# Kernel tuning notes

Hardware: AMD Instinct MI355X
Metric: run time of the kernel (lower is better)

## Reference

```python
import jax, jax.numpy as jnp
import numpy as np

B, S, D, H = 4, 2048, 1024, 16
DK = D // H


def setup_inputs() -> dict:
    key = jax.random.key(0)
    kx, kq, kk, kv, ko = jax.random.split(key, 5)
    scale = D ** -0.5
    return {
        "x": jax.random.normal(kx, (B, S, D), dtype=jnp.float32),
        "W_q": jax.random.normal(kq, (D, D), dtype=jnp.float32) * scale,
        "W_k": jax.random.normal(kk, (D, D), dtype=jnp.float32) * scale,
        "W_v": jax.random.normal(kv, (D, D), dtype=jnp.float32) * scale,
        "W_o": jax.random.normal(ko, (D, D), dtype=jnp.float32) * scale,
    }


def reference(x, W_q, W_k, W_v, W_o):
    b, s, d = x.shape
    # projections: x @ W.T  (weights stored [out, in])
    def proj(W):
        return (x @ W.T).reshape(b, s, H, DK).transpose(0, 2, 1, 3)  # [b,h,s,dk]
    Q, K, V = proj(W_q), proj(W_k), proj(W_v)
    scores = jnp.einsum('bhqd,bhkd->bhqk', Q, K) * (DK ** -0.5)
    causal = jnp.tril(jnp.ones((s, s), dtype=bool))
    scores = jnp.where(causal, scores, -jnp.inf)
    attn = jax.nn.softmax(scores, axis=-1)
    out = jnp.einsum('bhqk,bhkd->bhqd', attn, V)  # [b,h,s,dk]
    out = out.transpose(0, 2, 1, 3).reshape(b, s, d)
    return out @ W_o.T
```

## Files before the change

kernel.cpp:

```cpp
#include <hip/hip_runtime.h>
#include <stdint.h>

#define B_ 4
#define S_ 2048
#define D_ 1024
#define H_ 16
#define DK_ 64
#define M_ (B_*S_)

typedef __attribute__((ext_vector_type(8))) short bhalf8;
typedef __attribute__((ext_vector_type(4))) short bhalf4;
typedef __attribute__((ext_vector_type(4))) float floatx4;
typedef unsigned short bfu;
typedef unsigned int u32;

__device__ __forceinline__ bfu f2bf(float f) {
  union { float f; u32 u; } v; v.f = f;
  u32 r = v.u + 0x7FFFu + ((v.u >> 16) & 1u);
  return (bfu)(r >> 16);
}

__device__ __forceinline__ u32 cvtpk(float a, float b) {
  u32 r;
  asm("v_cvt_pk_bf16_f32 %0, %1, %2" : "=v"(r) : "v"(a), "v"(b));
  return r;
}

__device__ __forceinline__ void gll16(const bfu* g, bfu* l) {
  __builtin_amdgcn_global_load_lds((__attribute__((address_space(1))) void*)g,
                                   (__attribute__((address_space(3))) void*)l,
                                   16, 0, 0);
}

__global__ void cvt_all(const float* __restrict__ x,  const float* __restrict__ wq,
                        const float* __restrict__ wk, const float* __restrict__ wv,
                        const float* __restrict__ wo, bfu* __restrict__ dst) {
  const size_t u = ((size_t)blockIdx.x * blockDim.x + threadIdx.x) * 4;
  const size_t XN = (size_t)M_ * D_;
  const float* src;
  if (u < XN) {
    src = x + u;
  } else {
    const size_t v = u - XN;
    const int wsel = (int)(v >> 20);
    const size_t off = v & ((size_t)(1u << 20) - 1);
    src = ((wsel == 0) ? wq : (wsel == 1) ? wk : (wsel == 2) ? wv : wo) + off;
  }
  float4 vv = *(const float4*)src;
  ushort4 o;
  o.x = f2bf(vv.x); o.y = f2bf(vv.y); o.z = f2bf(vv.z); o.w = f2bf(vv.w);
  *(ushort4*)(dst + u) = o;
}

__device__ __forceinline__ void gemm_core_gll(const bfu* __restrict__ A,
                                              const bfu* __restrict__ Bw,
                                              bfu* aT, bfu* bT,
                                              int m0, int bn0,
                                              floatx4 (&acc)[4][4])
{
  const int tid  = threadIdx.x;
  const int lane = tid & 63;
  const int g    = lane >> 4;
  const int i16  = lane & 15;
  const int w    = tid >> 6;
  const int wm   = w >> 1, wn = w & 1;

  const int lrow = lane >> 3;
  const int scol = ((lane & 7) ^ lrow) << 3;
  const bfu* As = A  + (size_t)(m0  + w * 32 + lrow) * D_ + scol;
  const bfu* Bs = Bw + (size_t)(bn0 + w * 32 + lrow) * D_ + scol;

  for (int k0 = 0; k0 < D_; k0 += 64) {
#pragma unroll
    for (int j = 0; j < 4; ++j) {
      gll16(As + (size_t)j * 8 * D_ + k0, aT + (w * 4 + j) * 512);
      gll16(Bs + (size_t)j * 8 * D_ + k0, bT + (w * 4 + j) * 512);
    }
    __syncthreads();
    const char* aTc = (const char*)aT;
    const char* bTc = (const char*)bT;
#pragma unroll
    for (int kb = 0; kb < 2; ++kb) {
      bhalf8 af[4], bf[4];
#pragma unroll
      for (int f = 0; f < 4; ++f) {
        int arow = wm * 64 + f * 16 + i16;
        af[f] = *(const bhalf8*)(aTc + arow * 128 + ((kb * 64 + g * 16) ^ ((arow & 7) << 4)));
        int brow = wn * 64 + f * 16 + i16;
        bf[f] = *(const bhalf8*)(bTc + brow * 128 + ((kb * 64 + g * 16) ^ ((brow & 7) << 4)));
      }
#pragma unroll
      for (int fm = 0; fm < 4; ++fm)
#pragma unroll
        for (int fn = 0; fn < 4; ++fn)
          acc[fm][fn] = __builtin_amdgcn_mfma_f32_16x16x32_bf16(af[fm], bf[fn], acc[fm][fn], 0, 0, 0);
    }
    __syncthreads();
  }
}

__global__ __launch_bounds__(256) void qkv_gemm(const bfu* __restrict__ xb,
                                                const bfu* __restrict__ wqkv,
                                                bfu* __restrict__ Qd,
                                                bfu* __restrict__ Kd,
                                                bfu* __restrict__ Vtd)
{
  __shared__ bfu aT[8192], bT[8192];
  const int bid = blockIdx.x;
  const int wi   = bid >> 3;
  const int xblk = wi >> 3;
  const int y    = ((bid & 7) << 3) | (wi & 7);
  const int m0   = y * 128;
  const int z    = xblk >> 3;
  const int n0   = (xblk & 7) * 128;
  const int bn0  = xblk * 128;

  floatx4 acc[4][4] = {};
  gemm_core_gll(xb, wqkv, aT, bT, m0, bn0, acc);

  bfu* dst = (z == 0) ? Qd : (z == 1) ? Kd : Vtd;
  const int lane = threadIdx.x & 63;
  const int g = lane >> 4, i16 = lane & 15;
  const int w = threadIdx.x >> 6, wm = w >> 1, wn = w & 1;
#pragma unroll
  for (int fm = 0; fm < 4; ++fm) {
#pragma unroll
    for (int fn = 0; fn < 4; ++fn) {
      int col = n0 + wn * 64 + fn * 16 + i16;
      int h = col >> 6, dk = col & 63;
#pragma unroll
      for (int r = 0; r < 4; ++r) {
        int mrow = m0 + wm * 64 + fm * 16 + g * 4 + r;
        int b = mrow >> 11, s = mrow & (S_ - 1);
        size_t idx = (z == 2)
            ? ((size_t)((b * H_ + h) * DK_ + dk)) * S_ + s
            : ((size_t)((b * H_ + h) * S_ + s)) * DK_ + dk;
        dst[idx] = f2bf(acc[fm][fn][r]);
      }
    }
  }
}

__global__ __launch_bounds__(256) void out_gemm(const bfu* __restrict__ Ab,
                                                const bfu* __restrict__ wob,
                                                float* __restrict__ out)
{
  __shared__ bfu aT[8192], bT[8192];
  const int bid = blockIdx.x;
  const int wi   = bid >> 3;
  const int xblk = wi >> 3;
  const int y    = ((bid & 7) << 3) | (wi & 7);
  const int m0   = y * 128;
  const int n0   = xblk * 128;

  floatx4 acc[4][4] = {};
  gemm_core_gll(Ab, wob, aT, bT, m0, n0, acc);

  const int lane = threadIdx.x & 63;
  const int g = lane >> 4, i16 = lane & 15;
  const int w = threadIdx.x >> 6, wm = w >> 1, wn = w & 1;
#pragma unroll
  for (int fm = 0; fm < 4; ++fm)
#pragma unroll
    for (int fn = 0; fn < 4; ++fn) {
      int col = n0 + wn * 64 + fn * 16 + i16;
#pragma unroll
      for (int r = 0; r < 4; ++r) {
        int mrow = m0 + wm * 64 + fm * 16 + g * 4 + r;
        out[(size_t)mrow * D_ + col] = acc[fm][fn][r];
      }
    }
}

template<int BUF>
__device__ __forceinline__ void attn_tile(const char* smem, int t, int ntw, int qr,
                                          int koff0, int koff1, const int (&voff)[4],
                                          bhalf8 qa0, bhalf8 qa1, int g, int i16,
                                          floatx4 (&ot)[4], float& mC2, float& lp)
{
  const float C2 = 0.125f * 1.44269504f;
  floatx4 sa[4] = {};
#pragma unroll
  for (int cb = 0; cb < 4; ++cb) {
    bhalf8 kf0 = *(const bhalf8*)(smem + BUF + cb * 2048 + koff0);
    bhalf8 kf1 = *(const bhalf8*)(smem + BUF + cb * 2048 + koff1);
    sa[cb] = __builtin_amdgcn_mfma_f32_16x16x32_bf16(kf0, qa0, sa[cb], 0, 0, 0);
    sa[cb] = __builtin_amdgcn_mfma_f32_16x16x32_bf16(kf1, qa1, sa[cb], 0, 0, 0);
  }
  if (t == ntw - 1) {
    const int kv0 = t * 64;
#pragma unroll
    for (int cb = 0; cb < 4; ++cb)
#pragma unroll
      for (int r = 0; r < 4; ++r)
        if (kv0 + cb * 16 + g * 4 + r > qr + i16) sa[cb][r] = -3.0e38f;
  }
  float pm = sa[0][0];
#pragma unroll
  for (int cb = 0; cb < 4; ++cb)
#pragma unroll
    for (int r = 0; r < 4; ++r)
      pm = fmaxf(pm, sa[cb][r]);
  pm = fmaxf(pm, __shfl_xor(pm, 16));
  pm = fmaxf(pm, __shfl_xor(pm, 32));
  const float pmC2 = pm * C2;
  if (!__all(pmC2 - mC2 <= 8.0f)) {
    const float nmax = fmaxf(mC2, pmC2);
    const float al = exp2f(mC2 - nmax);
    mC2 = nmax;
    lp *= al;
#pragma unroll
    for (int da = 0; da < 4; ++da)
#pragma unroll
      for (int r = 0; r < 4; ++r)
        ot[da][r] *= al;
  }
  const float nm = -mC2;
  u32 pk[8];
  float ps = 0.f;
#pragma unroll
  for (int cb = 0; cb < 4; ++cb) {
    float p0 = exp2f(__builtin_fmaf(sa[cb][0], C2, nm));
    float p1 = exp2f(__builtin_fmaf(sa[cb][1], C2, nm));
    float p2 = exp2f(__builtin_fmaf(sa[cb][2], C2, nm));
    float p3 = exp2f(__builtin_fmaf(sa[cb][3], C2, nm));
    ps += (p0 + p1) + (p2 + p3);
    pk[cb * 2]     = cvtpk(p0, p1);
    pk[cb * 2 + 1] = cvtpk(p2, p3);
  }
  lp += ps;
#pragma unroll
  for (int da = 0; da < 4; ++da) {
#pragma unroll
    for (int cb = 0; cb < 4; ++cb) {
      bhalf4 vf = *(const bhalf4*)(smem + BUF + voff[cb] + da * 2048);
      union { u32 u[2]; bhalf4 h; } pu;
      pu.u[0] = pk[cb * 2]; pu.u[1] = pk[cb * 2 + 1];
      ot[da] = __builtin_amdgcn_mfma_f32_16x16x16bf16_1k(vf, pu.h, ot[da], 0, 0, 0);
    }
  }
}

__global__ __launch_bounds__(512, 4) void attn_kernel(const bfu* __restrict__ Q,
                                                      const bfu* __restrict__ Kc,
                                                      const bfu* __restrict__ Vt,
                                                      bfu* __restrict__ Oc)
{
  __shared__ char smem[2 * 16384];
  const int tid = threadIdx.x;
  const int lane = tid & 63;
  const int w = tid >> 6;
  const int g = lane >> 4, i16 = lane & 15;
  const int sw = (i16 & 7) << 4;
  const int bh = blockIdx.x;
  const int y0 = blockIdx.y;

  const bfu* Qb = Q  + (size_t)bh * S_ * DK_;
  const bfu* Kb = Kc + (size_t)bh * S_ * DK_;
  const bfu* Vb = Vt + (size_t)bh * DK_ * S_;
  const int b = bh >> 4, h = bh & 15;

  const int srow = tid >> 3;
  const int scolb = (tid & 7) * 16;
  const bfu* kgp = Kb + srow * DK_ + (scolb >> 1);
  const bfu* vgp = Vb + (size_t)srow * S_ + (scolb >> 1);
  char* kld = smem + srow * 128 + (scolb ^ ((srow & 7) << 4));
  const int vsw = ((srow & 7) << 4) | (srow & 8);
  char* vld0 = smem + 8192 + srow * 128 + ((scolb    ) ^ vsw);
  char* vld1 = smem + 8192 + srow * 128 + ((scolb + 8) ^ vsw);

  const int koff0 = i16 * 128 + ((g * 16) ^ sw);
  const int koff1 = i16 * 128 + ((64 + g * 16) ^ sw);
  const int vswr = sw | (i16 & 8);
  int voff[4];
#pragma unroll
  for (int cb = 0; cb < 4; ++cb)
    voff[cb] = 8192 + i16 * 128 + ((cb * 32 + g * 8) ^ vswr);

  for (int pass = 0; pass < 2; ++pass) {
    const int y = pass ? (15 - y0) : y0;
    const int ntw = 2 * y + 1 + (w >> 2);
    const int qr = y * 128 + w * 16;
    const int spine = 2 * y + 2;

    bhalf8 qa0 = *(const bhalf8*)(Qb + (size_t)(qr + i16) * DK_ + g * 8);
    bhalf8 qa1 = *(const bhalf8*)(Qb + (size_t)(qr + i16) * DK_ + 32 + g * 8);

    floatx4 ot[4] = {};
    float mC2 = -1.0e30f;
    float lp  = 0.f;

    union { bhalf8 h8; bhalf4 h4[2]; } vu;
    bhalf8 kst = *(const bhalf8*)kgp;
    bhalf8 vst = *(const bhalf8*)vgp;
    *(bhalf8*)kld = kst;
    vu.h8 = vst;
    *(bhalf4*)vld0 = vu.h4[0]; *(bhalf4*)vld1 = vu.h4[1];
    __syncthreads();

    const int half = spine >> 1;
    for (int i = 0; ; ++i) {
      const int t0 = 2 * i, t1 = 2 * i + 1;
      const bool more = (i + 1 < half);
      kst = *(const bhalf8*)(kgp + (size_t)t1 * 4096);
      vst = *(const bhalf8*)(vgp + t1 * 64);
      if (t0 < ntw)
        attn_tile<0>(smem, t0, ntw, qr, koff0, koff1, voff, qa0, qa1, g, i16, ot, mC2, lp);
      *(bhalf8*)(kld + 16384) = kst;
      vu.h8 = vst;
      *(bhalf4*)(vld0 + 16384) = vu.h4[0]; *(bhalf4*)(vld1 + 16384) = vu.h4[1];
      __syncthreads();
      if (more) {
        kst = *(const bhalf8*)(kgp + (size_t)(t0 + 2) * 4096);
        vst = *(const bhalf8*)(vgp + (t0 + 2) * 64);
      }
      if (t1 < ntw)
        attn_tile<16384>(smem, t1, ntw, qr, koff0, koff1, voff, qa0, qa1, g, i16, ot, mC2, lp);
      if (!more) break;
      *(bhalf8*)kld = kst;
      vu.h8 = vst;
      *(bhalf4*)vld0 = vu.h4[0]; *(bhalf4*)vld1 = vu.h4[1];
      __syncthreads();
    }
    __syncthreads();

    float lt = lp;
    lt += __shfl_xor(lt, 16);
    lt += __shfl_xor(lt, 32);
    const float rl = 1.0f / lt;
    const size_t rowbase = (size_t)(b * S_ + qr + i16) * D_ + h * 64;
#pragma unroll
    for (int da = 0; da < 4; ++da) {
      union { u32 u[2]; uint2 v; } ov;
      ov.u[0] = cvtpk(ot[da][0] * rl, ot[da][1] * rl);
      ov.u[1] = cvtpk(ot[da][2] * rl, ot[da][3] * rl);
      *(uint2*)(Oc + rowbase + da * 16 + g * 4) = ov.v;
    }
  }
}

extern "C" void kernel_launch(void* const* d_in, const int* in_sizes, int n_in,
                              void* d_out, int out_size, void* d_ws, size_t ws_size,
                              hipStream_t stream)
{
  const float* x  = (const float*)d_in[0];
  const float* wq = (const float*)d_in[1];
  const float* wk = (const float*)d_in[2];
  const float* wv = (const float*)d_in[3];
  const float* wo = (const float*)d_in[4];

  bfu* xb  = (bfu*)d_ws;
  bfu* wqb = xb  + (size_t)M_ * D_;
  bfu* wob = wqb + (size_t)3 * D_ * D_;
  bfu* Qd  = wob + (size_t)D_ * D_;
  bfu* Kd  = Qd  + (size_t)M_ * D_;
  bfu* Vtd = Kd  + (size_t)M_ * D_;
  bfu* Ad  = Vtd + (size_t)M_ * D_;

  const size_t total = (size_t)M_ * D_ + 4 * (size_t)D_ * D_;
  cvt_all<<<(int)(total / 4 / 256), 256, 0, stream>>>(x, wq, wk, wv, wo, xb);

  qkv_gemm<<<1536, 256, 0, stream>>>(xb, wqb, Qd, Kd, Vtd);
  attn_kernel<<<dim3(B_ * H_, 8), 512, 0, stream>>>(Qd, Kd, Vtd, Ad);
  out_gemm<<<512, 256, 0, stream>>>(Ad, wob, (float*)d_out);
}
```

Baseline: 177.4 us.

## Pipeline projection GEMMs with a four-stage LDS ring buffer

```diff
diff --git a/kernel.cpp b/kernel.cpp
--- a/kernel.cpp
+++ b/kernel.cpp
@@ -52,11 +52,11 @@
   *(ushort4*)(dst + u) = o;
 }
 
-__device__ __forceinline__ void gemm_core_gll(const bfu* __restrict__ A,
-                                              const bfu* __restrict__ Bw,
-                                              bfu* aT, bfu* bT,
-                                              int m0, int bn0,
-                                              floatx4 (&acc)[4][4])
+__device__ __forceinline__ void gemm_core_ring(const bfu* __restrict__ A,
+                                               const bfu* __restrict__ Bw,
+                                               bfu* smem,
+                                               int m0, int bn0,
+                                               floatx4 (&acc)[4][4])
 {
   const int tid  = threadIdx.x;
   const int lane = tid & 63;
@@ -69,16 +69,23 @@
   const int scol = ((lane & 7) ^ lrow) << 3;
   const bfu* As = A  + (size_t)(m0  + w * 32 + lrow) * D_ + scol;
   const bfu* Bs = Bw + (size_t)(bn0 + w * 32 + lrow) * D_ + scol;
-
-  for (int k0 = 0; k0 < D_; k0 += 64) {
-#pragma unroll
-    for (int j = 0; j < 4; ++j) {
-      gll16(As + (size_t)j * 8 * D_ + k0, aT + (w * 4 + j) * 512);
-      gll16(Bs + (size_t)j * 8 * D_ + k0, bT + (w * 4 + j) * 512);
-    }
-    __syncthreads();
-    const char* aTc = (const char*)aT;
-    const char* bTc = (const char*)bT;
+  const int ldst = w * 4 * 512;
+
+  auto STAGE = [&](int t) {
+    bfu* base = smem + (t & 3) * 16384;
+    const int k0 = t * 64;
+#pragma unroll
+    for (int j = 0; j < 4; ++j)
+      gll16(As + (size_t)j * 8 * D_ + k0, base + ldst + j * 512);
+#pragma unroll
+    for (int j = 0; j < 4; ++j)
+      gll16(Bs + (size_t)j * 8 * D_ + k0, base + 8192 + ldst + j * 512);
+  };
+
+  auto COMPUTE = [&](int t) {
+    const char* aTc = (const char*)(smem + (t & 3) * 16384);
+    const char* bTc = aTc + 16384;
+    __builtin_amdgcn_s_setprio(1);
 #pragma unroll
     for (int kb = 0; kb < 2; ++kb) {
       bhalf8 af[4], bf[4];
@@ -95,8 +102,28 @@
         for (int fn = 0; fn < 4; ++fn)
           acc[fm][fn] = __builtin_amdgcn_mfma_f32_16x16x32_bf16(af[fm], bf[fn], acc[fm][fn], 0, 0, 0);
     }
-    __syncthreads();
-  }
+    __builtin_amdgcn_s_setprio(0);
+  };
+
+  STAGE(0); STAGE(1); STAGE(2);
+  asm volatile("s_waitcnt vmcnt(16)" ::: "memory");
+  __builtin_amdgcn_s_barrier();
+  for (int t = 0; t < 13; ++t) {
+    STAGE(t + 3);
+    COMPUTE(t);
+    __builtin_amdgcn_sched_barrier(0);
+    asm volatile("s_waitcnt vmcnt(16)" ::: "memory");
+    __builtin_amdgcn_s_barrier();
+  }
+  COMPUTE(13);
+  __builtin_amdgcn_sched_barrier(0);
+  asm volatile("s_waitcnt vmcnt(8)" ::: "memory");
+  __builtin_amdgcn_s_barrier();
+  COMPUTE(14);
+  __builtin_amdgcn_sched_barrier(0);
+  asm volatile("s_waitcnt vmcnt(0)" ::: "memory");
+  __builtin_amdgcn_s_barrier();
+  COMPUTE(15);
 }
 
 __global__ __launch_bounds__(256) void qkv_gemm(const bfu* __restrict__ xb,
@@ -105,7 +132,7 @@
                                                 bfu* __restrict__ Kd,
                                                 bfu* __restrict__ Vtd)
 {
-  __shared__ bfu aT[8192], bT[8192];
+  __shared__ bfu smem[4 * 16384];
   const int bid = blockIdx.x;
   const int wi   = bid >> 3;
   const int xblk = wi >> 3;
@@ -116,7 +143,7 @@
   const int bn0  = xblk * 128;
 
   floatx4 acc[4][4] = {};
-  gemm_core_gll(xb, wqkv, aT, bT, m0, bn0, acc);
+  gemm_core_ring(xb, wqkv, smem, m0, bn0, acc);
 
   bfu* dst = (z == 0) ? Qd : (z == 1) ? Kd : Vtd;
   const int lane = threadIdx.x & 63;
@@ -145,7 +172,7 @@
                                                 const bfu* __restrict__ wob,
                                                 float* __restrict__ out)
 {
-  __shared__ bfu aT[8192], bT[8192];
+  __shared__ bfu smem[4 * 16384];
   const int bid = blockIdx.x;
   const int wi   = bid >> 3;
   const int xblk = wi >> 3;
@@ -154,7 +181,7 @@
   const int n0   = xblk * 128;
 
   floatx4 acc[4][4] = {};
-  gemm_core_gll(Ab, wob, aT, bT, m0, n0, acc);
+  gemm_core_ring(Ab, wob, smem, m0, n0, acc);
 
   const int lane = threadIdx.x & 63;
   const int g = lane >> 4, i16 = lane & 15;
```

After: 202.4 us. 1.14x slower.

## Enlarge projection GEMM tiles to 256x256 with double-buffered LDS prefetch

Applied to the files above, without the earlier changes.

```diff
diff --git a/kernel.cpp b/kernel.cpp
--- a/kernel.cpp
+++ b/kernel.cpp
@@ -52,85 +52,146 @@
   *(ushort4*)(dst + u) = o;
 }
 
-__device__ __forceinline__ void gemm_core_gll(const bfu* __restrict__ A,
+__device__ __forceinline__ void gemm_core_256(const bfu* __restrict__ A,
                                               const bfu* __restrict__ Bw,
-                                              bfu* aT, bfu* bT,
+                                              bfu* smem,
                                               int m0, int bn0,
-                                              floatx4 (&acc)[4][4])
+                                              floatx4 (&acc)[8][4])
 {
   const int tid  = threadIdx.x;
   const int lane = tid & 63;
   const int g    = lane >> 4;
   const int i16  = lane & 15;
   const int w    = tid >> 6;
-  const int wm   = w >> 1, wn = w & 1;
-
-  const int lrow = lane >> 3;
-  const int scol = ((lane & 7) ^ lrow) << 3;
-  const bfu* As = A  + (size_t)(m0  + w * 32 + lrow) * D_ + scol;
-  const bfu* Bs = Bw + (size_t)(bn0 + w * 32 + lrow) * D_ + scol;
-
-  for (int k0 = 0; k0 < D_; k0 += 64) {
-#pragma unroll
-    for (int j = 0; j < 4; ++j) {
-      gll16(As + (size_t)j * 8 * D_ + k0, aT + (w * 4 + j) * 512);
-      gll16(Bs + (size_t)j * 8 * D_ + k0, bT + (w * 4 + j) * 512);
-    }
+  const int wm   = w >> 2;
+  const int wn   = w & 3;
+
+  const int srow8 = lane >> 3;
+  const int scole = ((lane & 7) ^ srow8) << 3;
+  const bfu* Ag = A  + (size_t)(m0  + w * 8 + srow8) * D_ + scole;
+  const bfu* Bg = Bw + (size_t)(bn0 + w * 8 + srow8) * D_ + scole;
+  const int ldw = (w * 8) * 64;
+
+  auto stageA = [&](int t, int h) {
+    bfu* dst = smem + (t & 1) * 32768 + (h * 128) * 64 + ldw;
+    const size_t go = (size_t)(h * 128) * D_ + t * 64;
+    gll16(Ag + go, dst);
+    gll16(Ag + go + (size_t)64 * D_, dst + 64 * 64);
+  };
+  auto stageB = [&](int t, int h) {
+    bfu* dst = smem + (t & 1) * 32768 + 16384 + (h * 128) * 64 + ldw;
+    const size_t go = (size_t)(h * 128) * D_ + t * 64;
+    gll16(Bg + go, dst);
+    gll16(Bg + go + (size_t)64 * D_, dst + 64 * 64);
+  };
+
+  stageA(0, 0); stageA(0, 1); stageB(0, 0); stageB(0, 1);
+  __syncthreads();
+
+  for (int t = 0; t < 16; ++t) {
+    const char* aTc = (const char*)(smem + (t & 1) * 32768);
+    const char* bTc = aTc + 32768;
+    const bool more = (t + 1 < 16);
+    bhalf8 af[4], bf[4];
+
+    if (more) { stageA(t + 1, 0); stageA(t + 1, 1); }
+#pragma unroll
+    for (int f = 0; f < 4; ++f) {
+      int brow = wn * 64 + f * 16 + i16;
+      bf[f] = *(const bhalf8*)(bTc + brow * 128 + ((g * 16) ^ ((brow & 7) << 4)));
+      int arow = wm * 128 + f * 16 + i16;
+      af[f] = *(const bhalf8*)(aTc + arow * 128 + ((g * 16) ^ ((arow & 7) << 4)));
+    }
+    __builtin_amdgcn_s_setprio(1);
+#pragma unroll
+    for (int fm = 0; fm < 4; ++fm)
+#pragma unroll
+      for (int fn = 0; fn < 4; ++fn)
+        acc[fm][fn] = __builtin_amdgcn_mfma_f32_16x16x32_bf16(af[fm], bf[fn], acc[fm][fn], 0, 0, 0);
+    __builtin_amdgcn_s_setprio(0);
+    __builtin_amdgcn_s_barrier();
+
+    if (more) { stageB(t + 1, 0); stageB(t + 1, 1); }
+#pragma unroll
+    for (int f = 0; f < 4; ++f) {
+      int arow = wm * 128 + (4 + f) * 16 + i16;
+      af[f] = *(const bhalf8*)(aTc + arow * 128 + ((g * 16) ^ ((arow & 7) << 4)));
+    }
+    __builtin_amdgcn_s_setprio(1);
+#pragma unroll
+    for (int fm = 0; fm < 4; ++fm)
+#pragma unroll
+      for (int fn = 0; fn < 4; ++fn)
+        acc[4 + fm][fn] = __builtin_amdgcn_mfma_f32_16x16x32_bf16(af[fm], bf[fn], acc[4 + fm][fn], 0, 0, 0);
+    __builtin_amdgcn_s_setprio(0);
+    __builtin_amdgcn_s_barrier();
+
+#pragma unroll
+    for (int f = 0; f < 4; ++f) {
+      int brow = wn * 64 + f * 16 + i16;
+      bf[f] = *(const bhalf8*)(bTc + brow * 128 + ((64 + g * 16) ^ ((brow & 7) << 4)));
+      int arow = wm * 128 + f * 16 + i16;
+      af[f] = *(const bhalf8*)(aTc + arow * 128 + ((64 + g * 16) ^ ((arow & 7) << 4)));
+    }
+    __builtin_amdgcn_s_setprio(1);
+#pragma unroll
+    for (int fm = 0; fm < 4; ++fm)
+#pragma unroll
+      for (int fn = 0; fn < 4; ++fn)
+        acc[fm][fn] = __builtin_amdgcn_mfma_f32_16x16x32_bf16(af[fm], bf[fn], acc[fm][fn], 0, 0, 0);
+    __builtin_amdgcn_s_setprio(0);
+    __builtin_amdgcn_s_barrier();
+
+#pragma unroll
+    for (int f = 0; f < 4; ++f) {
+      int arow = wm * 128 + (4 + f) * 16 + i16;
+      af[f] = *(const bhalf8*)(aTc + arow * 128 + ((64 + g * 16) ^ ((arow & 7) << 4)));
+    }
+    __builtin_amdgcn_s_setprio(1);
+#pragma unroll
+    for (int fm = 0; fm < 4; ++fm)
+#pragma unroll
+      for (int fn = 0; fn < 4; ++fn)
+        acc[4 + fm][fn] = __builtin_amdgcn_mfma_f32_16x16x32_bf16(af[fm], bf[fn], acc[4 + fm][fn], 0, 0, 0);
+    __builtin_amdgcn_s_setprio(0);
     __syncthreads();
-    const char* aTc = (const char*)aT;
-    const char* bTc = (const char*)bT;
-#pragma unroll
-    for (int kb = 0; kb < 2; ++kb) {
-      bhalf8 af[4], bf[4];
-#pragma unroll
-      for (int f = 0; f < 4; ++f) {
-        int arow = wm * 64 + f * 16 + i16;
-        af[f] = *(const bhalf8*)(aTc + arow * 128 + ((kb * 64 + g * 16) ^ ((arow & 7) << 4)));
-        int brow = wn * 64 + f * 16 + i16;
-        bf[f] = *(const bhalf8*)(bTc + brow * 128 + ((kb * 64 + g * 16) ^ ((brow & 7) << 4)));
-      }
-#pragma unroll
-      for (int fm = 0; fm < 4; ++fm)
-#pragma unroll
-        for (int fn = 0; fn < 4; ++fn)
-          acc[fm][fn] = __builtin_amdgcn_mfma_f32_16x16x32_bf16(af[fm], bf[fn], acc[fm][fn], 0, 0, 0);
-    }
-    __syncthreads();
-  }
-}
-
-__global__ __launch_bounds__(256) void qkv_gemm(const bfu* __restrict__ xb,
-                                                const bfu* __restrict__ wqkv,
-                                                bfu* __restrict__ Qd,
-                                                bfu* __restrict__ Kd,
-                                                bfu* __restrict__ Vtd)
-{
-  __shared__ bfu aT[8192], bT[8192];
-  const int bid = blockIdx.x;
-  const int wi   = bid >> 3;
-  const int xblk = wi >> 3;
-  const int y    = ((bid & 7) << 3) | (wi & 7);
-  const int m0   = y * 128;
-  const int z    = xblk >> 3;
-  const int n0   = (xblk & 7) * 128;
-  const int bn0  = xblk * 128;
-
-  floatx4 acc[4][4] = {};
-  gemm_core_gll(xb, wqkv, aT, bT, m0, bn0, acc);
+  }
+}
+
+__global__ __launch_bounds__(512, 2) void qkv_gemm(const bfu* __restrict__ xb,
+                                                   const bfu* __restrict__ wqkv,
+                                                   bfu* __restrict__ Qd,
+                                                   bfu* __restrict__ Kd,
+                                                   bfu* __restrict__ Vtd)
+{
+  extern __shared__ bfu smem[];
+  const int bid  = blockIdx.x;
+  const int c    = bid & 7;
+  const int rr   = bid >> 3;
+  const int msub = rr & 3;
+  const int nblk = rr >> 2;
+  const int y    = c * 4 + msub;
+  const int m0   = y * 256;
+  const int bn0  = nblk * 256;
+  const int z    = bn0 >> 10;
+  const int n0   = bn0 & 1023;
+
+  floatx4 acc[8][4] = {};
+  gemm_core_256(xb, wqkv, smem, m0, bn0, acc);
 
   bfu* dst = (z == 0) ? Qd : (z == 1) ? Kd : Vtd;
   const int lane = threadIdx.x & 63;
   const int g = lane >> 4, i16 = lane & 15;
-  const int w = threadIdx.x >> 6, wm = w >> 1, wn = w & 1;
-#pragma unroll
-  for (int fm = 0; fm < 4; ++fm) {
+  const int w = threadIdx.x >> 6, wm = w >> 2, wn = w & 3;
+#pragma unroll
+  for (int fm = 0; fm < 8; ++fm) {
 #pragma unroll
     for (int fn = 0; fn < 4; ++fn) {
       int col = n0 + wn * 64 + fn * 16 + i16;
       int h = col >> 6, dk = col & 63;
 #pragma unroll
       for (int r = 0; r < 4; ++r) {
-        int mrow = m0 + wm * 64 + fm * 16 + g * 4 + r;
+        int mrow = m0 + wm * 128 + fm * 16 + g * 4 + r;
         int b = mrow >> 11, s = mrow & (S_ - 1);
         size_t idx = (z == 2)
             ? ((size_t)((b * H_ + h) * DK_ + dk)) * S_ + s
@@ -141,32 +202,34 @@
   }
 }
 
-__global__ __launch_bounds__(256) void out_gemm(const bfu* __restrict__ Ab,
-                                                const bfu* __restrict__ wob,
-                                                float* __restrict__ out)
-{
-  __shared__ bfu aT[8192], bT[8192];
-  const int bid = blockIdx.x;
-  const int wi   = bid >> 3;
-  const int xblk = wi >> 3;
-  const int y    = ((bid & 7) << 3) | (wi & 7);
-  const int m0   = y * 128;
-  const int n0   = xblk * 128;
-
-  floatx4 acc[4][4] = {};
-  gemm_core_gll(Ab, wob, aT, bT, m0, n0, acc);
+__global__ __launch_bounds__(512, 2) void out_gemm(const bfu* __restrict__ Ab,
+                                                   const bfu* __restrict__ wob,
+                                                   float* __restrict__ out)
+{
+  extern __shared__ bfu smem[];
+  const int bid  = blockIdx.x;
+  const int c    = bid & 7;
+  const int rr   = bid >> 3;
+  const int msub = rr & 3;
+  const int nblk = rr >> 2;
+  const int y    = c * 4 + msub;
+  const int m0   = y * 256;
+  const int n0   = nblk * 256;
+
+  floatx4 acc[8][4] = {};
+  gemm_core_256(Ab, wob, smem, m0, n0, acc);
 
   const int lane = threadIdx.x & 63;
   const int g = lane >> 4, i16 = lane & 15;
-  const int w = threadIdx.x >> 6, wm = w >> 1, wn = w & 1;
-#pragma unroll
-  for (int fm = 0; fm < 4; ++fm)
+  const int w = threadIdx.x >> 6, wm = w >> 2, wn = w & 3;
+#pragma unroll
+  for (int fm = 0; fm < 8; ++fm)
 #pragma unroll
     for (int fn = 0; fn < 4; ++fn) {
       int col = n0 + wn * 64 + fn * 16 + i16;
 #pragma unroll
       for (int r = 0; r < 4; ++r) {
-        int mrow = m0 + wm * 64 + fm * 16 + g * 4 + r;
+        int mrow = m0 + wm * 128 + fm * 16 + g * 4 + r;
         out[(size_t)mrow * D_ + col] = acc[fm][fn][r];
       }
     }
@@ -357,10 +420,15 @@
   bfu* Vtd = Kd  + (size_t)M_ * D_;
   bfu* Ad  = Vtd + (size_t)M_ * D_;
 
+  (void)hipFuncSetAttribute((const void*)qkv_gemm,
+                            hipFuncAttributeMaxDynamicSharedMemorySize, 131072);
+  (void)hipFuncSetAttribute((const void*)out_gemm,
+                            hipFuncAttributeMaxDynamicSharedMemorySize, 131072);
+
   const size_t total = (size_t)M_ * D_ + 4 * (size_t)D_ * D_;
   cvt_all<<<(int)(total / 4 / 256), 256, 0, stream>>>(x, wq, wk, wv, wo, xb);
 
-  qkv_gemm<<<1536, 256, 0, stream>>>(xb, wqb, Qd, Kd, Vtd);
+  qkv_gemm<<<384, 512, 131072, stream>>>(xb, wqb, Qd, Kd, Vtd);
   attn_kernel<<<dim3(B_ * H_, 8), 512, 0, stream>>>(Qd, Kd, Vtd, Ad);
-  out_gemm<<<512, 256, 0, stream>>>(Ad, wob, (float*)d_out);
-}
+  out_gemm<<<128, 512, 131072, stream>>>(Ad, wob, (float*)d_out);
+}
```

Result: slower. 195.2 us (+10.1%).
